# Kernel optimization log

Hardware: AMD Instinct MI355X
Metric: run time of the kernel (lower is better)

Reference implementation:

```python
import jax, jax.numpy as jnp
import numpy as np

HIDDEN = 1024
HEADS = 16
HEAD_DIM = HIDDEN // HEADS
LN_EPS = 1e-12


def _layer_norm(x, gamma, beta, eps=LN_EPS):
    mu = jnp.mean(x, axis=-1, keepdims=True)
    var = jnp.var(x, axis=-1, keepdims=True)
    return (x - mu) * jax.lax.rsqrt(var + eps) * gamma + beta


def setup_inputs() -> dict:
    key = jax.random.key(0)
    ks = jax.random.split(key, 8)
    B, S = 4, 2048
    hidden_states = jax.random.normal(ks[0], (B, S, HIDDEN), dtype=jnp.float32)
    attention_mask = jnp.zeros((B, 1, 1, S), dtype=jnp.float32)
    scale = 1.0 / np.sqrt(HIDDEN)
    return {
        "hidden_states": hidden_states,
        "attention_mask": attention_mask,
        "ln_gamma": jnp.ones((HIDDEN,), jnp.float32),
        "ln_beta": jnp.zeros((HIDDEN,), jnp.float32),
        "W_qkv": jax.random.normal(ks[1], (HIDDEN, 3 * HIDDEN), jnp.float32) * scale,
        "b_qkv": jnp.zeros((3 * HIDDEN,), jnp.float32),
        "W_out": jax.random.normal(ks[2], (HIDDEN, HIDDEN), jnp.float32) * scale,
        "b_out": jnp.zeros((HIDDEN,), jnp.float32),
    }


def reference(hidden_states, attention_mask, ln_gamma, ln_beta, W_qkv, b_qkv, W_out, b_out):
    B, S, H = hidden_states.shape
    x = _layer_norm(hidden_states, ln_gamma, ln_beta)
    qkv = x @ W_qkv + b_qkv  # [B, S, 3H]
    q, k, v = jnp.split(qkv, 3, axis=-1)
    q = q.reshape(B, S, HEADS, HEAD_DIM)
    k = k.reshape(B, S, HEADS, HEAD_DIM)
    v = v.reshape(B, S, HEADS, HEAD_DIM)
    # scores: [B, heads, q_len, kv_len]
    scores = jnp.einsum("bqhd,bkhd->bhqk", q, k) * (1.0 / np.sqrt(HEAD_DIM))
    scores = scores + attention_mask
    probs = jax.nn.softmax(scores, axis=-1)
    attn = jnp.einsum("bhqk,bkhd->bqhd", probs, v).reshape(B, S, H)
    out = attn @ W_out + b_out
    out = out + hidden_states  # residual (dropout is identity at p=0)
    return out
```

## Files before the change

kernel.cpp:

```cpp
#include <hip/hip_runtime.h>

#define SEQ 2048
#define HID 1024
#define NHEAD 16
#define HDIM 64
#define NB 4
#define NTOK (NB * SEQ)
#define NQKV (3 * HID)
#define LOG2E 1.44269504088896f
#define QSCALE (0.125f * LOG2E)

typedef __attribute__((ext_vector_type(8))) short bf16x8;
typedef __attribute__((ext_vector_type(4))) float f32x4;


__device__ __forceinline__ void glds16(const void* g, void* l) {
  __builtin_amdgcn_global_load_lds(
      (const __attribute__((address_space(1))) void*)g,
      (__attribute__((address_space(3))) void*)l, 16, 0, 0);
}

__device__ __forceinline__ ushort f2bf(float f) {
  union { float f; unsigned int u; } a; a.f = f;
  unsigned int u = a.u;
  return (ushort)((u + 0x7fffu + ((u >> 16) & 1u)) >> 16);
}

__device__ __forceinline__ unsigned int cvtpk(float a, float b) {
  unsigned int r;
  asm("v_cvt_pk_bf16_f32 %0, %1, %2" : "=v"(r) : "v"(a), "v"(b));
  return r;
}


__global__ __launch_bounds__(256) void ln_kernel(const float* __restrict__ x,
                                                 const float* __restrict__ g,
                                                 const float* __restrict__ be,
                                                 ushort* __restrict__ y) {
  const int row = blockIdx.x;
  const int tid = threadIdx.x;
  const float4 v = ((const float4*)(x + (size_t)row * HID))[tid];
  float s  = v.x + v.y + v.z + v.w;
  float sq = v.x * v.x + v.y * v.y + v.z * v.z + v.w * v.w;
  for (int o = 1; o < 64; o <<= 1) { s += __shfl_xor(s, o, 64); sq += __shfl_xor(sq, o, 64); }
  __shared__ float as_[4], aq_[4];
  const int wv = tid >> 6;
  if ((tid & 63) == 0) { as_[wv] = s; aq_[wv] = sq; }
  __syncthreads();
  s  = as_[0] + as_[1] + as_[2] + as_[3];
  sq = aq_[0] + aq_[1] + aq_[2] + aq_[3];
  const float mu  = s * (1.0f / HID);
  const float var = sq * (1.0f / HID) - mu * mu;
  const float rs  = rsqrtf(var + 1e-12f);
  const float4 gv = ((const float4*)g)[tid];
  const float4 bv = ((const float4*)be)[tid];
  ushort4 o;
  o.x = f2bf((v.x - mu) * rs * gv.x + bv.x);
  o.y = f2bf((v.y - mu) * rs * gv.y + bv.y);
  o.z = f2bf((v.z - mu) * rs * gv.z + bv.z);
  o.w = f2bf((v.w - mu) * rs * gv.w + bv.w);
  ((ushort4*)(y + (size_t)row * HID))[tid] = o;
}


__global__ __launch_bounds__(256) void transpose_cvt2(const float* __restrict__ W0,
                                                      ushort* __restrict__ T0,
                                                      const float* __restrict__ W1,
                                                      ushort* __restrict__ T1) {
  const float* W; ushort* WT; int C;
  if (blockIdx.z == 0) { W = W0; WT = T0; C = NQKV; }
  else { if (blockIdx.x >= HID / 32) return; W = W1; WT = T1; C = HID; }
  const int R = HID;
  __shared__ float t[32][33];
  const int c0 = blockIdx.x * 32, r0 = blockIdx.y * 32;
  const int tx = threadIdx.x & 31, ty = threadIdx.x >> 5;
  for (int j = 0; j < 4; ++j)
    t[ty + j * 8][tx] = W[(size_t)(r0 + ty + j * 8) * C + c0 + tx];
  __syncthreads();
  for (int j = 0; j < 4; ++j)
    WT[(size_t)(c0 + ty + j * 8) * R + r0 + tx] = f2bf(t[tx][ty + j * 8]);
}


__global__ __launch_bounds__(256) void v_transpose(const ushort* __restrict__ qkv,
                                                   ushort* __restrict__ vt) {
  __shared__ ushort t[64][66];
  const int s0 = blockIdx.x * 64, h = blockIdx.y, b = blockIdx.z;
  const size_t tokbase = (size_t)b * SEQ;
  for (int e = 0; e < 2; ++e) {
    const int c = e * 256 + threadIdx.x;
    const int sr = c >> 3, dc = c & 7;
    *(uint4*)&t[sr][dc * 8] =
        *(const uint4*)(qkv + (tokbase + s0 + sr) * NQKV + 2 * HID + h * HDIM + dc * 8);
  }
  __syncthreads();
  for (int e = 0; e < 2; ++e) {
    const int c = e * 256 + threadIdx.x;
    const int dr = c >> 3, sc = c & 7;
    ushort tmp[8];
    for (int j = 0; j < 8; ++j) tmp[j] = t[sc * 8 + j][dr];
    *(uint4*)(vt + ((size_t)(b * NHEAD + h) * HDIM + dr) * SEQ + s0 + sc * 8) = *(uint4*)tmp;
  }
}


template <int MODE>
__global__ __launch_bounds__(256) void gemm_bt(const ushort* __restrict__ A,
                                               const ushort* __restrict__ Bt,
                                               const float* __restrict__ bias,
                                               const float* __restrict__ resid,
                                               ushort* __restrict__ obf,
                                               float* __restrict__ of32,
                                               int M, int N, int K) {
  __shared__ ushort As[128 * 64];
  __shared__ ushort Bs[128 * 64];
  const int tid = threadIdx.x;
  const int lane = tid & 63, wv = tid >> 6;
  const int q = lane >> 4, li = lane & 15;
  const int m0 = blockIdx.y * 128, n0 = blockIdx.x * 128;
  const int wm = (wv >> 1) * 64, wn = (wv & 1) * 64;
  f32x4 acc[4][4] = {};

  for (int kb = 0; kb < K; kb += 64) {
    for (int e = 0; e < 4; ++e) {
      const int chunk = (wv * 4 + e) * 64 + lane;
      const int row = chunk >> 3, slot = chunk & 7;
      const int kc = slot ^ (row & 7);
      glds16(A  + (size_t)(m0 + row) * K + kb + kc * 8, As + (wv * 4 + e) * 512);
      glds16(Bt + (size_t)(n0 + row) * K + kb + kc * 8, Bs + (wv * 4 + e) * 512);
    }
    __syncthreads();
    for (int ks = 0; ks < 2; ++ks) {
      const int kc = ks * 4 + q;
      bf16x8 af[4], bfr[4];
      for (int mi = 0; mi < 4; ++mi) {
        const int row = wm + mi * 16 + li;
        af[mi] = *(const bf16x8*)(As + (row * 8 + (kc ^ (row & 7))) * 8);
      }
      for (int ni = 0; ni < 4; ++ni) {
        const int row = wn + ni * 16 + li;
        bfr[ni] = *(const bf16x8*)(Bs + (row * 8 + (kc ^ (row & 7))) * 8);
      }
      for (int mi = 0; mi < 4; ++mi)
        for (int ni = 0; ni < 4; ++ni)
          acc[mi][ni] = __builtin_amdgcn_mfma_f32_16x16x32_bf16(af[mi], bfr[ni], acc[mi][ni], 0, 0, 0);
    }
    __syncthreads();
  }

  const float qs = (MODE == 0 && n0 < HID) ? QSCALE : 1.0f;
  for (int ni = 0; ni < 4; ++ni) {
    const int col = n0 + wn + ni * 16 + li;
    const float bvs = bias[col] * qs;
    for (int mi = 0; mi < 4; ++mi) {
      for (int r = 0; r < 4; ++r) {
        const int row = m0 + wm + mi * 16 + q * 4 + r;
        const float v = fmaf(acc[mi][ni][r], qs, bvs);
        if (MODE == 0) obf[(size_t)row * N + col] = f2bf(v);
        else           of32[(size_t)row * N + col] = v + resid[(size_t)row * N + col];
      }
    }
  }
}


__global__ __launch_bounds__(256) void flash_attn(const ushort* __restrict__ qkv,
                                                  const ushort* __restrict__ vt,
                                                  const float* __restrict__ mask,
                                                  ushort* __restrict__ outa) {
  __shared__ ushort KV[2][8192];
  const int tid = threadIdx.x, lane = tid & 63, wv = tid >> 6;
  const int quad = lane >> 4, li = lane & 15;
  const int wq = wv * 32;
  constexpr int NT = SEQ / 64;

  const int L = blockIdx.x + 16 * blockIdx.y + 256 * blockIdx.z;
  const int xcd = L & 7, rrem = L >> 3;
  const int p = (rrem >> 4) * 8 + xcd;
  const int qt = rrem & 15, h = p & 15, b = p >> 4;

  const size_t tokbase = (size_t)b * SEQ;
  const size_t vtbase = (size_t)(b * NHEAD + h) * HDIM * SEQ;
  const float* mrow = mask + (size_t)b * SEQ;

  for (int e = 0; e < 4; ++e) {
    const int c = (wv * 4 + e) * 64 + lane;
    const int row = c >> 3, slot = c & 7;
    const int kc = slot ^ (row & 7);
    glds16(qkv + (tokbase + qt * 128 + row) * NQKV + h * HDIM + kc * 8,
           &KV[0][0] + (wv * 4 + e) * 512);
  }
  __syncthreads();

  bf16x8 qf[2][2];
  for (int ks = 0; ks < 2; ++ks) {
    const int kc = ks * 4 + quad;
    for (int nq = 0; nq < 2; ++nq) {
      const int row = wq + nq * 16 + li;
      qf[ks][nq] = *(const bf16x8*)(&KV[0][0] + (row * 8 + (kc ^ (row & 7))) * 8);
    }
  }
  __syncthreads();

  int koff[2][4], voff[2][4];
  for (int ks = 0; ks < 2; ++ks) {
    const int kc = ks * 4 + quad;
    for (int i = 0; i < 4; ++i) {
      const int row = i * 16 + li;
      koff[ks][i] = (row * 8 + (kc ^ (row & 7))) * 8;
      voff[ks][i] = koff[ks][i] + 4096;
    }
  }
  unsigned ksoff[2], vsoff[2];
  for (int e = 0; e < 2; ++e) {
    const int c = (wv * 2 + e) * 64 + lane;
    const int row = c >> 3, slot = c & 7;
    const int kc = slot ^ (row & 7);
    const int gkv = (row & 0x23) | ((row & 0x0c) << 1) | ((row & 0x10) >> 2);
    ksoff[e] = (unsigned)((tokbase + gkv) * NQKV + HID + h * HDIM + kc * 8);
    vsoff[e] = (unsigned)(vtbase + (size_t)row * SEQ + kc * 8);
  }

  const unsigned int one2 = 0x3F803F80u;
  bf16x8 ones;
  for (int j = 0; j < 4; ++j) ((unsigned int*)&ones)[j] = one2;

  f32x4 accO[2][4] = {};
  f32x4 accL[2] = {};

  auto stage_kv = [&](int t, int buf) {
    const unsigned ka = (unsigned)(t * (64 * NQKV));
    const unsigned va = (unsigned)(t * 64);
    for (int e = 0; e < 2; ++e) {
      glds16(qkv + ksoff[e] + ka, &KV[buf][0] + (wv * 2 + e) * 512);
      glds16(vt + vsoff[e] + va,  &KV[buf][4096] + (wv * 2 + e) * 512);
    }
  };

  auto mask_fetch = [&](int t, float4 (&mk)[4]) {
    const int kv0 = (t & (NT - 1)) * 64;
    for (int m = 0; m < 4; ++m) {
      const float4 v = *(const float4*)(mrow + kv0 + (m >> 1) * 32 + quad * 8 + (m & 1) * 4);
      mk[m].x = v.x * LOG2E; mk[m].y = v.y * LOG2E;
      mk[m].z = v.z * LOG2E; mk[m].w = v.w * LOG2E;
    }
  };

  auto compute = [&](int t, int buf, float4 (&mkc)[4], float4 (&mkn)[4]) {
    mask_fetch(t + 1, mkn);

    const ushort* Kb = &KV[buf][0];

    f32x4 cin[4];
    for (int m = 0; m < 4; ++m)
      cin[m] = (f32x4){mkc[m].x, mkc[m].y, mkc[m].z, mkc[m].w};

    f32x4 sc[2][4];
    __builtin_amdgcn_s_setprio(1);
    for (int ks = 0; ks < 2; ++ks) {
      bf16x8 kf[4];
      for (int m = 0; m < 4; ++m)
        kf[m] = *(const bf16x8*)(Kb + koff[ks][m]);
      for (int nq = 0; nq < 2; ++nq)
        for (int m = 0; m < 4; ++m)
          sc[nq][m] = __builtin_amdgcn_mfma_f32_16x16x32_bf16(
              kf[m], qf[ks][nq], ks == 0 ? cin[m] : sc[nq][m], 0, 0, 0);
    }
    __builtin_amdgcn_s_setprio(0);

    for (int ks = 0; ks < 2; ++ks) {
      bf16x8 vf[4];
      for (int nd = 0; nd < 4; ++nd)
        vf[nd] = *(const bf16x8*)(Kb + voff[ks][nd]);
      unsigned int pk[2][2][2];
      for (int nq = 0; nq < 2; ++nq)
        for (int mm = 0; mm < 2; ++mm) {
          const int m = 2 * ks + mm;
          const float p0 = __builtin_amdgcn_exp2f(sc[nq][m][0]);
          const float p1 = __builtin_amdgcn_exp2f(sc[nq][m][1]);
          const float p2 = __builtin_amdgcn_exp2f(sc[nq][m][2]);
          const float p3 = __builtin_amdgcn_exp2f(sc[nq][m][3]);
          pk[nq][mm][0] = cvtpk(p0, p1);
          pk[nq][mm][1] = cvtpk(p2, p3);
        }
      __builtin_amdgcn_s_setprio(1);
      for (int mq = 0; mq < 2; ++mq) {
        bf16x8 pf;
        ((unsigned int*)&pf)[0] = pk[mq][0][0];
        ((unsigned int*)&pf)[1] = pk[mq][0][1];
        ((unsigned int*)&pf)[2] = pk[mq][1][0];
        ((unsigned int*)&pf)[3] = pk[mq][1][1];
        for (int nd = 0; nd < 4; ++nd)
          accO[mq][nd] = __builtin_amdgcn_mfma_f32_16x16x32_bf16(pf, vf[nd], accO[mq][nd], 0, 0, 0);
        accL[mq] = __builtin_amdgcn_mfma_f32_16x16x32_bf16(pf, ones, accL[mq], 0, 0, 0);
      }
      __builtin_amdgcn_s_setprio(0);
    }
  };

  float4 mkA[4], mkB[4];
  mask_fetch(0, mkA);
  stage_kv(0, 0);
  for (int t = 0; t < NT; t += 2) {
    __syncthreads();
    stage_kv(t + 1, 1);
    compute(t, 0, mkA, mkB);
    __syncthreads();
    if (t + 2 < SEQ / 64) stage_kv(t + 2, 0);
    compute(t + 1, 1, mkB, mkA);
  }

  for (int mq = 0; mq < 2; ++mq)
    for (int r = 0; r < 4; ++r) {
      const float inv = 1.0f / accL[mq][r];
      const size_t tok = tokbase + qt * 128 + wq + mq * 16 + quad * 4 + r;
      for (int nd = 0; nd < 4; ++nd)
        outa[tok * HID + h * HDIM + nd * 16 + li] = f2bf(accO[mq][nd][r] * inv);
    }
}


extern "C" void kernel_launch(void* const* d_in, const int* in_sizes, int n_in,
                              void* d_out, int out_size, void* d_ws, size_t ws_size,
                              hipStream_t stream) {
  const float* hidden = (const float*)d_in[0];
  const float* mask   = (const float*)d_in[1];
  const float* gamma  = (const float*)d_in[2];
  const float* beta   = (const float*)d_in[3];
  const float* Wqkv   = (const float*)d_in[4];
  const float* bqkv   = (const float*)d_in[5];
  const float* Wout   = (const float*)d_in[6];
  const float* bout   = (const float*)d_in[7];
  float* out = (float*)d_out;

  char* ws = (char*)d_ws;
  ushort* x_bf  = (ushort*)(ws);
  ushort* vtb   = (ushort*)(ws);
  ushort* wqkvT = (ushort*)(ws + ((size_t)16 << 20));
  ushort* woutT = (ushort*)(ws + ((size_t)22 << 20));
  ushort* qkvb  = (ushort*)(ws + ((size_t)24 << 20));
  ushort* attnb = (ushort*)(ws + ((size_t)72 << 20));

  ln_kernel<<<NTOK, 256, 0, stream>>>(hidden, gamma, beta, x_bf);
  transpose_cvt2<<<dim3(NQKV / 32, HID / 32, 2), 256, 0, stream>>>(Wqkv, wqkvT, Wout, woutT);
  gemm_bt<0><<<dim3(NQKV / 128, NTOK / 128), 256, 0, stream>>>(
      x_bf, wqkvT, bqkv, nullptr, qkvb, nullptr, NTOK, NQKV, HID);
  v_transpose<<<dim3(SEQ / 64, NHEAD, NB), 256, 0, stream>>>(qkvb, vtb);
  flash_attn<<<dim3(SEQ / 128, NHEAD, NB), 256, 0, stream>>>(qkvb, vtb, mask, attnb);
  gemm_bt<1><<<dim3(HID / 128, NTOK / 128), 256, 0, stream>>>(
      attnb, woutT, bout, hidden, nullptr, out, NTOK, HID, HID);
}
```

Baseline: 299.2 us.

## Rewrite bf16 GEMM as 256x256-tile double-buffered pipelined kernel with 512 threads

Replaces the 128x128, single-buffered GEMM with a 256x256 tile, 8-wave kernel. It uses double-buffered LDS and issues global-to-LDS prefetches of the next K tiles, interleaved across four MFMA phases with explicit vmcnt waits, barriers and setprio. The aim is to hide global load latency and raise the number of MFMAs per LDS byte. The trade-off is far fewer blocks: 384 for the QKV GEMM and only 128 for the output projection, which risks idle CUs and wave-quantization losses. The 128KB of LDS per block also limits each CU to one block.

Result: slower. 320.6 us (+7.2%).

```diff
diff --git a/kernel.cpp b/kernel.cpp
--- a/kernel.cpp
+++ b/kernel.cpp
@@ -105,57 +105,143 @@
 
 
 template <int MODE>
-__global__ __launch_bounds__(256) void gemm_bt(const ushort* __restrict__ A,
-                                               const ushort* __restrict__ Bt,
-                                               const float* __restrict__ bias,
-                                               const float* __restrict__ resid,
-                                               ushort* __restrict__ obf,
-                                               float* __restrict__ of32,
-                                               int M, int N, int K) {
-  __shared__ ushort As[128 * 64];
-  __shared__ ushort Bs[128 * 64];
+__global__ __launch_bounds__(512, 2) void gemm_bt(const ushort* __restrict__ Ag,
+                                                  const ushort* __restrict__ Bg,
+                                                  const float* __restrict__ bias,
+                                                  const float* __restrict__ resid,
+                                                  ushort* __restrict__ obf,
+                                                  float* __restrict__ of32,
+                                                  int M, int N, int K) {
+  __shared__ ushort lds[65536];
   const int tid = threadIdx.x;
   const int lane = tid & 63, wv = tid >> 6;
-  const int q = lane >> 4, li = lane & 15;
-  const int m0 = blockIdx.y * 128, n0 = blockIdx.x * 128;
-  const int wm = (wv >> 1) * 64, wn = (wv & 1) * 64;
-  f32x4 acc[4][4] = {};
-
-  for (int kb = 0; kb < K; kb += 64) {
-    for (int e = 0; e < 4; ++e) {
-      const int chunk = (wv * 4 + e) * 64 + lane;
-      const int row = chunk >> 3, slot = chunk & 7;
-      const int kc = slot ^ (row & 7);
-      glds16(A  + (size_t)(m0 + row) * K + kb + kc * 8, As + (wv * 4 + e) * 512);
-      glds16(Bt + (size_t)(n0 + row) * K + kb + kc * 8, Bs + (wv * 4 + e) * 512);
-    }
-    __syncthreads();
-    for (int ks = 0; ks < 2; ++ks) {
-      const int kc = ks * 4 + q;
-      bf16x8 af[4], bfr[4];
-      for (int mi = 0; mi < 4; ++mi) {
-        const int row = wm + mi * 16 + li;
-        af[mi] = *(const bf16x8*)(As + (row * 8 + (kc ^ (row & 7))) * 8);
-      }
-      for (int ni = 0; ni < 4; ++ni) {
-        const int row = wn + ni * 16 + li;
-        bfr[ni] = *(const bf16x8*)(Bs + (row * 8 + (kc ^ (row & 7))) * 8);
-      }
-      for (int mi = 0; mi < 4; ++mi)
-        for (int ni = 0; ni < 4; ++ni)
-          acc[mi][ni] = __builtin_amdgcn_mfma_f32_16x16x32_bf16(af[mi], bfr[ni], acc[mi][ni], 0, 0, 0);
-    }
-    __syncthreads();
-  }
+  const int quad = lane >> 4, li = lane & 15;
+  const int wm2 = wv >> 2, wn4 = wv & 3;
+  const int m0 = blockIdx.y * 256, n0 = blockIdx.x * 256;
+  const int NKT = K >> 6;
+
+  auto stageA = [&](int kt, int u) {
+    const int db = (kt & 1) * 16384;
+    const size_t kb = (size_t)kt * 64;
+    const int rin = tid >> 3;
+    const int kc = (tid & 7) ^ (rin & 7);
+#pragma unroll
+    for (int e = 0; e < 2; ++e) {
+      const int gr = m0 + e * 128 + u * 64 + rin;
+      glds16(Ag + (size_t)gr * K + kb + kc * 8,
+             lds + db + ((u * 2 + e) * 64 + wv * 8) * 64);
+    }
+  };
+  auto stageB = [&](int kt, int u) {
+    const int db = (kt & 1) * 16384;
+    const size_t kb = (size_t)kt * 64;
+    const int rin = tid >> 3;
+    const int kc = (tid & 7) ^ (rin & 7);
+#pragma unroll
+    for (int e = 0; e < 2; ++e) {
+      const int s = 2 * e + (rin >> 5);
+      const int gr = n0 + s * 64 + u * 32 + (rin & 31);
+      glds16(Bg + (size_t)gr * K + kb + kc * 8,
+             lds + 32768 + db + ((u * 4 + 2 * e + (wv >> 2)) * 32 + (wv & 3) * 8) * 64);
+    }
+  };
+
+  int arow[2][4], brow[2][2], soff[2];
+#pragma unroll
+  for (int mh = 0; mh < 2; ++mh)
+#pragma unroll
+    for (int i = 0; i < 4; ++i)
+      arow[mh][i] = ((mh * 2 + wm2) * 64 + i * 16 + li) * 64;
+#pragma unroll
+  for (int u = 0; u < 2; ++u)
+#pragma unroll
+    for (int j = 0; j < 2; ++j)
+      brow[u][j] = ((u * 4 + wn4) * 32 + j * 16 + li) * 64;
+#pragma unroll
+  for (int ks = 0; ks < 2; ++ks)
+    soff[ks] = ((ks * 4 + quad) ^ (li & 7)) * 8;
+
+  f32x4 acc[8][4] = {};
+  bf16x8 af[4][2], bfr[2][2];
+
+#define GPHASE(MH, NH)                                                        \
+  __builtin_amdgcn_s_barrier();                                               \
+  asm volatile("s_waitcnt lgkmcnt(0)");                                       \
+  __builtin_amdgcn_s_setprio(1);                                              \
+  _Pragma("unroll") for (int ks = 0; ks < 2; ++ks)                            \
+      _Pragma("unroll") for (int i = 0; i < 4; ++i)                           \
+          _Pragma("unroll") for (int j = 0; j < 2; ++j)                       \
+              acc[(MH)*4 + i][(NH)*2 + j] =                                   \
+                  __builtin_amdgcn_mfma_f32_16x16x32_bf16(                    \
+                      af[i][ks], bfr[j][ks], acc[(MH)*4 + i][(NH)*2 + j],     \
+                      0, 0, 0);                                               \
+  __builtin_amdgcn_s_setprio(0);
+
+  stageA(0, 0); stageB(0, 1); stageA(0, 1); stageB(0, 0);
+  stageA(1, 0); stageB(1, 1);
+  asm volatile("s_waitcnt vmcnt(4)" ::: "memory");
+  __builtin_amdgcn_s_barrier();
+  asm volatile("" ::: "memory");
+
+  for (int k = 0; k < NKT; ++k) {
+    const ushort* Ab = lds + (k & 1) * 16384;
+    const ushort* Bb = lds + 32768 + (k & 1) * 16384;
+#pragma unroll
+    for (int i = 0; i < 4; ++i)
+#pragma unroll
+      for (int ks = 0; ks < 2; ++ks)
+        af[i][ks] = *(const bf16x8*)(Ab + arow[0][i] + soff[ks]);
+#pragma unroll
+    for (int j = 0; j < 2; ++j)
+#pragma unroll
+      for (int ks = 0; ks < 2; ++ks)
+        bfr[j][ks] = *(const bf16x8*)(Bb + brow[0][j] + soff[ks]);
+    if (k + 1 < NKT) stageA(k + 1, 1);
+    GPHASE(0, 0)
+    __builtin_amdgcn_s_barrier();
+#pragma unroll
+    for (int j = 0; j < 2; ++j)
+#pragma unroll
+      for (int ks = 0; ks < 2; ++ks)
+        bfr[j][ks] = *(const bf16x8*)(Bb + brow[1][j] + soff[ks]);
+    if (k + 1 < NKT) stageB(k + 1, 0);
+    GPHASE(0, 1)
+    __builtin_amdgcn_s_barrier();
+#pragma unroll
+    for (int i = 0; i < 4; ++i)
+#pragma unroll
+      for (int ks = 0; ks < 2; ++ks)
+        af[i][ks] = *(const bf16x8*)(Ab + arow[1][i] + soff[ks]);
+    if (k + 2 < NKT) stageA(k + 2, 0);
+    GPHASE(1, 1)
+    __builtin_amdgcn_s_barrier();
+#pragma unroll
+    for (int j = 0; j < 2; ++j)
+#pragma unroll
+      for (int ks = 0; ks < 2; ++ks)
+        bfr[j][ks] = *(const bf16x8*)(Bb + brow[0][j] + soff[ks]);
+    if (k + 2 < NKT) stageB(k + 2, 1);
+    GPHASE(1, 0)
+    if (k + 1 < NKT) {
+      if (k + 2 < NKT) asm volatile("s_waitcnt vmcnt(4)" ::: "memory");
+      else             asm volatile("s_waitcnt vmcnt(0)" ::: "memory");
+    }
+    __builtin_amdgcn_s_barrier();
+    asm volatile("" ::: "memory");
+  }
+#undef GPHASE
 
   const float qs = (MODE == 0 && n0 < HID) ? QSCALE : 1.0f;
-  for (int ni = 0; ni < 4; ++ni) {
-    const int col = n0 + wn + ni * 16 + li;
+#pragma unroll
+  for (int nf = 0; nf < 4; ++nf) {
+    const int col = n0 + wn4 * 64 + nf * 16 + li;
     const float bvs = bias[col] * qs;
-    for (int mi = 0; mi < 4; ++mi) {
+#pragma unroll
+    for (int mf = 0; mf < 8; ++mf) {
+#pragma unroll
       for (int r = 0; r < 4; ++r) {
-        const int row = m0 + wm + mi * 16 + q * 4 + r;
-        const float v = fmaf(acc[mi][ni][r], qs, bvs);
+        const int row = m0 + wm2 * 128 + mf * 16 + quad * 4 + r;
+        const float v = fmaf(acc[mf][nf][r], qs, bvs);
         if (MODE == 0) obf[(size_t)row * N + col] = f2bf(v);
         else           of32[(size_t)row * N + col] = v + resid[(size_t)row * N + col];
       }
@@ -343,10 +429,10 @@
 
   ln_kernel<<<NTOK, 256, 0, stream>>>(hidden, gamma, beta, x_bf);
   transpose_cvt2<<<dim3(NQKV / 32, HID / 32, 2), 256, 0, stream>>>(Wqkv, wqkvT, Wout, woutT);
-  gemm_bt<0><<<dim3(NQKV / 128, NTOK / 128), 256, 0, stream>>>(
+  gemm_bt<0><<<dim3(NQKV / 256, NTOK / 256), 512, 0, stream>>>(
       x_bf, wqkvT, bqkv, nullptr, qkvb, nullptr, NTOK, NQKV, HID);
   v_transpose<<<dim3(SEQ / 64, NHEAD, NB), 256, 0, stream>>>(qkvb, vtb);
   flash_attn<<<dim3(SEQ / 128, NHEAD, NB), 256, 0, stream>>>(qkvb, vtb, mask, attnb);
-  gemm_bt<1><<<dim3(HID / 128, NTOK / 128), 256, 0, stream>>>(
+  gemm_bt<1><<<dim3(HID / 256, NTOK / 256), 512, 0, stream>>>(
       attnb, woutT, bout, hidden, nullptr, out, NTOK, HID, HID);
 }
```
